# Kernel tuning notes

Measured on AMD Instinct MI355X. Metric: run time of the kernel, lower is better.

Reference implementation:

```python
import jax, jax.numpy as jnp
import numpy as np

P, K, H, D = 64, 8, 32, 2048   # ids_per_batch, imgs_per_id, local stripes, feature dim
MARGIN = 10.0


def _euclid(x, y):
    # x: [m, d], y: [n, d] -> [m, n]
    xx = jnp.sum(x * x, axis=1, keepdims=True)          # [m, 1]
    yy = jnp.sum(y * y, axis=1)[None, :]                # [1, n]
    d2 = xx + yy - 2.0 * (x @ y.T)
    return jnp.sqrt(jnp.clip(d2, 1e-12, None))


def _shortest_dist(dmat):
    # dmat: [m, n, *rest]; DP: dist[i,j] = dmat[i,j] + min(dist[i-1,j], dist[i,j-1])
    m, n = dmat.shape[0], dmat.shape[1]
    rest = dmat.shape[2:]
    d = dmat.reshape(m, n, -1)                          # [m, n, B]
    B = d.shape[2]
    # virtual row above: +inf everywhere except col 0 (so dist[0,0] = dmat[0,0])
    prev0 = jnp.full((n, B), jnp.inf, d.dtype).at[0].set(0.0)

    def row_step(prev_row, drow):
        def col_step(left, ud):
            up, dd = ud
            cur = jnp.minimum(up, left) + dd
            return cur, cur
        _, row = jax.lax.scan(col_step, jnp.full((B,), jnp.inf, d.dtype), (prev_row, drow))
        return row, None

    last_row, _ = jax.lax.scan(row_step, prev0, d)
    return last_row[-1].reshape(rest)                   # dist at (m-1, n-1)


def _local_dist(x, y):
    # x: [M, m, d], y: [N, n, d] -> [M, N]
    M, m, d = x.shape
    N, n, _ = y.shape
    dm = _euclid(x.reshape(M * m, d), y.reshape(N * n, d))
    dm = jnp.tanh(dm * 0.5)                             # (e^d - 1) / (e^d + 1)
    dm = dm.reshape(M, m, N, n).transpose(1, 3, 0, 2)   # [m, n, M, N]
    return _shortest_dist(dm)                           # [M, N]


def setup_inputs() -> dict:
    key = jax.random.key(0)
    features = jax.random.normal(key, (P * K, H, D), dtype=jnp.float32)
    targets = jnp.arange(P * K, dtype=jnp.int32) // K   # ordered p*k labels
    return {"features": features, "targets": targets}


def reference(features, targets):
    # ordered p*k batch: classes are contiguous blocks of K
    feats = features.reshape(P, K, H, D)
    centers = feats.mean(axis=1)                        # [P, H, D]

    # intra: center vs its K members -> max over members, per class
    intra_max = jax.vmap(lambda c, f: _local_dist(c[None], f).max())(centers, feats)  # [P]

    # inter: center vs all other centers -> min over others, per class
    inter_full = _local_dist(centers, centers)          # [P, P]
    eye = jnp.eye(P, dtype=bool)
    inter_min = jnp.where(eye, jnp.inf, inter_full).min(axis=1)  # [P]

    loss = jnp.mean(jax.nn.relu(intra_max - inter_min + MARGIN))
    return loss, intra_max, inter_min
```

## Files before the change

kernel.cpp:

```cpp
#include <hip/hip_runtime.h>
#include <hip/hip_fp8.h>
#include <cstdint>
#include <cstddef>

#define PP 64
#define KK 8
#define HH 32
#define DD 2048
#define RR (PP*HH)

typedef __attribute__((ext_vector_type(4))) float  f32x4;
typedef __attribute__((ext_vector_type(4))) float  float4v;

__device__ __forceinline__ unsigned int f2fp8(float f) {
  return (unsigned int)__hip_fp8_e4m3(f).__x;
}

__device__ __forceinline__ void gload_lds16(const void* g, void* l) {
  __builtin_amdgcn_global_load_lds(
      (const __attribute__((address_space(1))) void*)g,
      (__attribute__((address_space(3))) void*)l, 16, 0, 0);
}

__device__ __forceinline__ void gload_lds16_nt(const void* g, void* l) {
  __builtin_amdgcn_global_load_lds(
      (const __attribute__((address_space(1))) void*)g,
      (__attribute__((address_space(3))) void*)l, 16, 0, 2);
}

__device__ __forceinline__ float dp_wave(const float* tile, int j32) {
  const float INF = __builtin_inff();
  float A = INF;
  for (int d = 0; d < 63; ++d) {
    float left = __shfl_up(A, 1, 32);
    if (j32 == 0) left = INF;
    int i = d - j32;
    int ii = i < 0 ? 0 : (i > 31 ? 31 : i);
    float dv = tile[(ii << 5) + j32];
    float up = (i == 0) ? (j32 == 0 ? 0.f : INF) : A;
    A = (i >= 0 && i < 32) ? (fminf(up, left) + dv) : INF;
  }
  return A;
}

__global__ __launch_bounds__(256) void k_centers(const float* __restrict__ feat,
    unsigned char* __restrict__ cbf, unsigned char* __restrict__ fbf,
    float* __restrict__ cnorm, float* __restrict__ fnorm) {
  int row = blockIdx.x;
  int p = row >> 5, h = row & 31;
  int tid = threadIdx.x;
  int d0 = tid * 8;
  float c[8];
  float red[9];
  #pragma unroll
  for (int e = 0; e < 8; ++e) c[e] = 0.f;
  #pragma unroll
  for (int k = 0; k < KK; ++k) {
    size_t frow = (size_t)((p*KK + k)*HH + h);
    const float* src = feat + frow*DD + d0;
    float4v f0 = *(const float4v*)src;
    float4v f1 = *(const float4v*)(src + 4);
    float s = 0.f;
    #pragma unroll
    for (int e = 0; e < 4; ++e) {
      c[e]   += f0[e];
      c[4+e] += f1[e];
      s += f0[e]*f0[e] + f1[e]*f1[e];
    }
    red[k] = s;
    unsigned int lo = f2fp8(f0[0]) | (f2fp8(f0[1])<<8) | (f2fp8(f0[2])<<16) | (f2fp8(f0[3])<<24);
    unsigned int hi = f2fp8(f1[0]) | (f2fp8(f1[1])<<8) | (f2fp8(f1[2])<<16) | (f2fp8(f1[3])<<24);
    *(uint2*)(fbf + frow*DD + d0) = make_uint2(lo, hi);
  }
  float csq = 0.f;
  #pragma unroll
  for (int e = 0; e < 8; ++e) { c[e] *= 0.125f; csq += c[e]*c[e]; }
  {
    unsigned int lo = f2fp8(c[0]) | (f2fp8(c[1])<<8) | (f2fp8(c[2])<<16) | (f2fp8(c[3])<<24);
    unsigned int hi = f2fp8(c[4]) | (f2fp8(c[5])<<8) | (f2fp8(c[6])<<16) | (f2fp8(c[7])<<24);
    *(uint2*)(cbf + (size_t)row*DD + d0) = make_uint2(lo, hi);
  }
  red[8] = csq;

  __shared__ float lred[4][9];
  int lane = tid & 63, wv = tid >> 6;
  #pragma unroll
  for (int r = 0; r < 9; ++r) {
    float v = red[r];
    #pragma unroll
    for (int off = 32; off > 0; off >>= 1) v += __shfl_down(v, off, 64);
    if (lane == 0) lred[wv][r] = v;
  }
  __syncthreads();
  if (tid < 9) {
    float s = lred[0][tid] + lred[1][tid] + lred[2][tid] + lred[3][tid];
    if (tid < 8) fnorm[((size_t)(p*KK + tid))*HH + h] = s;
    else         cnorm[row] = s;
  }
}

__global__ __launch_bounds__(256) void k_gram(const unsigned char* __restrict__ cbf,
    const unsigned char* __restrict__ fbf, const float* __restrict__ cnorm,
    const float* __restrict__ fnorm, float* __restrict__ inter_full,
    float* __restrict__ intra_pk) {
  __shared__ char smem[24576];
  int tid = threadIdx.x, lane = tid & 63, w = tid >> 6;
  int ln = lane & 15, kq = lane >> 4;
  int cch = (lane & 3) ^ ((lane >> 3) & 3);

  if (blockIdx.x < 528) {
    int bid = (blockIdx.x & 7)*66 + (blockIdx.x >> 3);
    int tI = 0, rem = bid;
    while (rem >= 32 - tI) { rem -= 32 - tI; ++tI; }
    int tJ = tI + rem;
    int wr = w >> 1, wc = w & 1;
    f32x4 acc[2][2];
    #pragma unroll
    for (int a = 0; a < 2; ++a)
      #pragma unroll
      for (int b = 0; b < 2; ++b)
        #pragma unroll
        for (int e = 0; e < 4; ++e) acc[a][b][e] = 0.f;

    const unsigned char* gA0 = cbf + (size_t)(tI*64 + w*16 + (lane >> 2))*DD + cch*16;
    const unsigned char* gB0 = cbf + (size_t)(tJ*64 + w*16 + (lane >> 2))*DD + cch*16;

    int aofs[2][2], bofs[2][2];
    #pragma unroll
    for (int ks = 0; ks < 2; ++ks) {
      int phys = ((ks*4 + kq) ^ (ln & 6))*8;
      #pragma unroll
      for (int mt = 0; mt < 2; ++mt) {
        aofs[ks][mt] = (wr*32 + mt*16 + ln)*64 + phys;
        bofs[ks][mt] = (wc*32 + mt*16 + ln)*64 + phys;
      }
    }

    auto stage = [&](int tt, int bi) {
      int k0 = tt * 64;
      char* A = smem + bi*8192;
      gload_lds16(gA0 + k0, A + w*1024 + lane*16);
      gload_lds16(gB0 + k0, A + 4096 + w*1024 + lane*16);
    };
    auto do_step = [&](int bi) {
      const char* A = smem + bi*8192;
      const char* B = A + 4096;
      #pragma unroll
      for (int ks = 0; ks < 2; ++ks) {
        long long af[2], bf[2];
        #pragma unroll
        for (int mt = 0; mt < 2; ++mt) {
          af[mt] = *(const long long*)(A + aofs[ks][mt]);
          bf[mt] = *(const long long*)(B + bofs[ks][mt]);
        }
        #pragma unroll
        for (int mt = 0; mt < 2; ++mt)
          #pragma unroll
          for (int nt = 0; nt < 2; ++nt)
            acc[mt][nt] = __builtin_amdgcn_mfma_f32_16x16x32_fp8_fp8(af[mt], bf[nt], acc[mt][nt], 0, 0, 0);
      }
    };

    stage(0, 0);
    stage(1, 1);
    asm volatile("s_waitcnt vmcnt(2)" ::: "memory");
    __builtin_amdgcn_s_barrier();
    for (int t = 0; t < 30; ++t) {
      stage(t + 2, (t + 2) % 3);
      do_step(t % 3);
      asm volatile("s_waitcnt vmcnt(2)" ::: "memory");
      __builtin_amdgcn_s_barrier();
    }
    do_step(0);
    asm volatile("s_waitcnt vmcnt(0)" ::: "memory");
    __builtin_amdgcn_s_barrier();
    do_step(1);
    __syncthreads();

    int a = tI*2 + wr, b = tJ*2 + wc;
    bool own = (a < b);
    float* tile = (float*)(smem + w*4096);
    if (own) {
      #pragma unroll
      for (int mt = 0; mt < 2; ++mt) {
        #pragma unroll
        for (int nt = 0; nt < 2; ++nt) {
          int j  = nt*16 + ln;
          int cc = tJ*64 + wc*32 + j;
          float nc = cnorm[cc];
          #pragma unroll
          for (int v = 0; v < 4; ++v) {
            int i  = mt*16 + kq*4 + v;
            int rr = tI*64 + wr*32 + i;
            float d2 = cnorm[rr] + nc - 2.f*acc[mt][nt][v];
            tile[(i << 5) + j] = tanhf(0.5f*sqrtf(fmaxf(d2, 1e-12f)));
          }
        }
      }
    }
    __syncthreads();
    if (own) {
      float A = dp_wave(tile, lane & 31);
      if (lane == 31) {
        inter_full[a*64 + b] = A;
        inter_full[b*64 + a] = A;
      }
    }
  } else {
    int bid = (int)blockIdx.x - 528;
    int p = bid >> 3, jb = bid & 7;
    int ks = w >> 1, nt = w & 1;
    f32x4 acc[2];
    #pragma unroll
    for (int mi = 0; mi < 2; ++mi)
      #pragma unroll
      for (int e = 0; e < 4; ++e) acc[mi][e] = 0.f;

    int hw = w & 1;
    const unsigned char* g0 = (w < 2)
        ? cbf + (size_t)(p*32 + hw*16 + (lane >> 2))*DD + cch*16
        : fbf + (size_t)(p*256 + jb*32 + hw*16 + (lane >> 2))*DD + cch*16;
    int isB = (w >= 2);

    int phys = ((ks*4 + kq) ^ (ln & 6))*8;
    int aofs[2];
    #pragma unroll
    for (int mi = 0; mi < 2; ++mi) aofs[mi] = (mi*16 + ln)*64 + phys;
    int bofs = (nt*16 + ln)*64 + phys;

    auto stage = [&](int tt, int bi) {
      int k0 = tt * 64;
      char* S = smem + bi*4096 + isB*2048;
      if (isB) gload_lds16_nt(g0 + k0, S + hw*1024 + lane*16);
      else     gload_lds16   (g0 + k0, S + hw*1024 + lane*16);
    };
    auto do_step = [&](int bi) {
      const char* A = smem + bi*4096;
      const char* B = A + 2048;
      long long bfr = *(const long long*)(B + bofs);
      #pragma unroll
      for (int mi = 0; mi < 2; ++mi) {
        long long af = *(const long long*)(A + aofs[mi]);
        acc[mi] = __builtin_amdgcn_mfma_f32_16x16x32_fp8_fp8(af, bfr, acc[mi], 0, 0, 0);
      }
    };

    stage(0, 0);
    stage(1, 1);
    asm volatile("s_waitcnt vmcnt(1)" ::: "memory");
    __builtin_amdgcn_s_barrier();
    for (int t = 0; t < 30; ++t) {
      stage(t + 2, (t + 2) % 3);
      do_step(t % 3);
      asm volatile("s_waitcnt vmcnt(1)" ::: "memory");
      __builtin_amdgcn_s_barrier();
    }
    do_step(0);
    asm volatile("s_waitcnt vmcnt(0)" ::: "memory");
    __builtin_amdgcn_s_barrier();
    do_step(1);

    float* fb = (float*)smem;
    float* tile = (float*)(smem + 16384);
    __syncthreads();
    if (w >= 2) {
      #pragma unroll
      for (int mi = 0; mi < 2; ++mi)
        *(f32x4*)(fb + ((w - 2)*2 + mi)*256 + lane*4) = acc[mi];
    }
    __syncthreads();
    if (w < 2) {
      #pragma unroll
      for (int mi = 0; mi < 2; ++mi)
        acc[mi] += *(const f32x4*)(fb + (w*2 + mi)*256 + lane*4);
      int cl = jb*32 + nt*16 + ln;
      float nf = fnorm[(size_t)p*256 + cl];
      #pragma unroll
      for (int mi = 0; mi < 2; ++mi) {
        #pragma unroll
        for (int v = 0; v < 4; ++v) {
          int i = mi*16 + kq*4 + v;
          float d2 = cnorm[p*32 + i] + nf - 2.f*acc[mi][v];
          tile[(i << 5) + (nt*16 + ln)] = tanhf(0.5f*sqrtf(fmaxf(d2, 1e-12f)));
        }
      }
    }
    __syncthreads();
    if (w == 0) {
      float A = dp_wave(tile, lane & 31);
      if (lane == 31) intra_pk[p*8 + jb] = A;
    }
  }
}

__global__ __launch_bounds__(64) void k_final(const float* __restrict__ inter_full,
    const float* __restrict__ intra_pk, float* __restrict__ out) {
  int p = threadIdx.x;
  const float INF = __builtin_inff();
  float mn = INF;
  #pragma unroll 8
  for (int b = 0; b < 64; ++b)
    if (b != p) mn = fminf(mn, inter_full[p*64 + b]);
  float mx = -INF;
  #pragma unroll
  for (int k = 0; k < 8; ++k) mx = fmaxf(mx, intra_pk[p*8 + k]);
  out[1 + p]  = mx;
  out[65 + p] = mn;
  float v = fmaxf(mx - mn + 10.0f, 0.0f);
  #pragma unroll
  for (int off = 32; off > 0; off >>= 1) v += __shfl_down(v, off, 64);
  if (p == 0) out[0] = v * (1.0f/64.0f);
}

extern "C" void kernel_launch(void* const* d_in, const int* in_sizes, int n_in,
                              void* d_out, int out_size, void* d_ws, size_t ws_size,
                              hipStream_t stream) {
  const float* feat = (const float*)d_in[0];
  float* out = (float*)d_out;
  char* w = (char*)d_ws;
  unsigned char* cbf  = (unsigned char*)w;
  unsigned char* fbf  = (unsigned char*)(w + 4194304);
  float* cnorm        = (float*)(w + 37748736);
  float* fnorm        = (float*)(w + 37756928);
  float* inter_full   = (float*)(w + 37822464);
  float* intra_pk     = (float*)(w + 37838848);

  k_centers<<<RR, 256, 0, stream>>>(feat, cbf, fbf, cnorm, fnorm);
  k_gram<<<1040, 256, 0, stream>>>(cbf, fbf, cnorm, fnorm, inter_full, intra_pk);
  k_final<<<1, 64, 0, stream>>>(inter_full, intra_pk, out);
}
```

Measured before the change: 73.11 us.

## Merge gram blocks into 512-thread blocks sharing the A tile across two column tiles

Each inter block now computes two adjacent column tiles (tJ pairs) in 512 threads, loading the row-tile A once into LDS and sharing it across both halves, so the amount of A data fetched from global memory drops. The intra blocks are also doubled up, each 512-thread block handling two (p, jb) jobs in separate LDS regions. The nontemporal load variant for feature data is dropped. The grid shrinks from 1040 to 528 blocks with a larger LDS footprint per block, which may reduce occupancy. Larger blocks also mean more waves waiting at each barrier.

```diff
diff --git a/kernel.cpp b/kernel.cpp
--- a/kernel.cpp
+++ b/kernel.cpp
@@ -20,12 +20,6 @@
   __builtin_amdgcn_global_load_lds(
       (const __attribute__((address_space(1))) void*)g,
       (__attribute__((address_space(3))) void*)l, 16, 0, 0);
-}
-
-__device__ __forceinline__ void gload_lds16_nt(const void* g, void* l) {
-  __builtin_amdgcn_global_load_lds(
-      (const __attribute__((address_space(1))) void*)g,
-      (__attribute__((address_space(3))) void*)l, 16, 0, 2);
 }
 
 __device__ __forceinline__ float dp_wave(const float* tile, int j32) {
@@ -99,21 +93,24 @@
   }
 }
 
-__global__ __launch_bounds__(256) void k_gram(const unsigned char* __restrict__ cbf,
+__global__ __launch_bounds__(512) void k_gram(const unsigned char* __restrict__ cbf,
     const unsigned char* __restrict__ fbf, const float* __restrict__ cnorm,
     const float* __restrict__ fnorm, float* __restrict__ inter_full,
     float* __restrict__ intra_pk) {
-  __shared__ char smem[24576];
+  __shared__ char smem[40960];
   int tid = threadIdx.x, lane = tid & 63, w = tid >> 6;
   int ln = lane & 15, kq = lane >> 4;
   int cch = (lane & 3) ^ ((lane >> 3) & 3);
 
-  if (blockIdx.x < 528) {
-    int bid = (blockIdx.x & 7)*66 + (blockIdx.x >> 3);
+  int xcd = blockIdx.x & 7, idx = blockIdx.x >> 3;
+  if (idx < 34) {
+    int bid = xcd*34 + idx;
     int tI = 0, rem = bid;
-    while (rem >= 32 - tI) { rem -= 32 - tI; ++tI; }
-    int tJ = tI + rem;
-    int wr = w >> 1, wc = w & 1;
+    while (rem >= 16 - (tI >> 1)) { rem -= 16 - (tI >> 1); ++tI; }
+    int tJp = (tI >> 1) + rem;
+    int jh = w >> 2, q = w & 3;
+    int wr = q >> 1, wc = q & 1;
+    int tJ = tJp*2 + jh;
     f32x4 acc[2][2];
     #pragma unroll
     for (int a = 0; a < 2; ++a)
@@ -122,8 +119,21 @@
         #pragma unroll
         for (int e = 0; e < 4; ++e) acc[a][b][e] = 0.f;
 
-    const unsigned char* gA0 = cbf + (size_t)(tI*64 + w*16 + (lane >> 2))*DD + cch*16;
-    const unsigned char* gB0 = cbf + (size_t)(tJ*64 + w*16 + (lane >> 2))*DD + cch*16;
+    const unsigned char* g0;
+    const unsigned char* g1 = nullptr;
+    int d0ofs = 0, d1ofs = 0;
+    int role2 = (w >= 4);
+    if (!role2) {
+      g0 = cbf + (size_t)(tI*64 + w*16 + (lane >> 2))*DD + cch*16;
+      d0ofs = w*1024 + lane*16;
+    } else {
+      int j = w - 4, jB = j >> 1, half = j & 1;
+      int tJj = tJp*2 + jB;
+      g0 = cbf + (size_t)(tJj*64 + half*32 + (lane >> 2))*DD + cch*16;
+      g1 = g0 + (size_t)16*DD;
+      d0ofs = 4096 + jB*4096 + half*2048 + lane*16;
+      d1ofs = d0ofs + 1024;
+    }
 
     int aofs[2][2], bofs[2][2];
     #pragma unroll
@@ -132,26 +142,25 @@
       #pragma unroll
       for (int mt = 0; mt < 2; ++mt) {
         aofs[ks][mt] = (wr*32 + mt*16 + ln)*64 + phys;
-        bofs[ks][mt] = (wc*32 + mt*16 + ln)*64 + phys;
+        bofs[ks][mt] = 4096 + jh*4096 + (wc*32 + mt*16 + ln)*64 + phys;
       }
     }
 
     auto stage = [&](int tt, int bi) {
       int k0 = tt * 64;
-      char* A = smem + bi*8192;
-      gload_lds16(gA0 + k0, A + w*1024 + lane*16);
-      gload_lds16(gB0 + k0, A + 4096 + w*1024 + lane*16);
+      char* buf = smem + bi*12288;
+      gload_lds16(g0 + k0, buf + d0ofs);
+      if (role2) gload_lds16(g1 + k0, buf + d1ofs);
     };
     auto do_step = [&](int bi) {
-      const char* A = smem + bi*8192;
-      const char* B = A + 4096;
+      const char* buf = smem + bi*12288;
       #pragma unroll
       for (int ks = 0; ks < 2; ++ks) {
         long long af[2], bf[2];
         #pragma unroll
         for (int mt = 0; mt < 2; ++mt) {
-          af[mt] = *(const long long*)(A + aofs[ks][mt]);
-          bf[mt] = *(const long long*)(B + bofs[ks][mt]);
+          af[mt] = *(const long long*)(buf + aofs[ks][mt]);
+          bf[mt] = *(const long long*)(buf + bofs[ks][mt]);
         }
         #pragma unroll
         for (int mt = 0; mt < 2; ++mt)
@@ -163,12 +172,14 @@
 
     stage(0, 0);
     stage(1, 1);
-    asm volatile("s_waitcnt vmcnt(2)" ::: "memory");
+    if (!role2) { asm volatile("s_waitcnt vmcnt(1)" ::: "memory"); }
+    else        { asm volatile("s_waitcnt vmcnt(2)" ::: "memory"); }
     __builtin_amdgcn_s_barrier();
     for (int t = 0; t < 30; ++t) {
       stage(t + 2, (t + 2) % 3);
       do_step(t % 3);
-      asm volatile("s_waitcnt vmcnt(2)" ::: "memory");
+      if (!role2) { asm volatile("s_waitcnt vmcnt(1)" ::: "memory"); }
+      else        { asm volatile("s_waitcnt vmcnt(2)" ::: "memory"); }
       __builtin_amdgcn_s_barrier();
     }
     do_step(0);
@@ -207,20 +218,24 @@
       }
     }
   } else {
-    int bid = (int)blockIdx.x - 528;
-    int p = bid >> 3, jb = bid & 7;
-    int ks = w >> 1, nt = w & 1;
+    int bid = xcd*32 + (idx - 34);
+    int u  = w >> 2;
+    int wu = w & 3;
+    int rb = u * 20480;
+    int qq = bid*2 + u;
+    int p = qq >> 3, jb = qq & 7;
+    int ks = wu >> 1, nt = wu & 1;
     f32x4 acc[2];
     #pragma unroll
     for (int mi = 0; mi < 2; ++mi)
       #pragma unroll
       for (int e = 0; e < 4; ++e) acc[mi][e] = 0.f;
 
-    int hw = w & 1;
-    const unsigned char* g0 = (w < 2)
+    int hw = wu & 1;
+    const unsigned char* g0 = (wu < 2)
         ? cbf + (size_t)(p*32 + hw*16 + (lane >> 2))*DD + cch*16
         : fbf + (size_t)(p*256 + jb*32 + hw*16 + (lane >> 2))*DD + cch*16;
-    int isB = (w >= 2);
+    int isB = (wu >= 2);
 
     int phys = ((ks*4 + kq) ^ (ln & 6))*8;
     int aofs[2];
@@ -230,12 +245,11 @@
 
     auto stage = [&](int tt, int bi) {
       int k0 = tt * 64;
-      char* S = smem + bi*4096 + isB*2048;
-      if (isB) gload_lds16_nt(g0 + k0, S + hw*1024 + lane*16);
-      else     gload_lds16   (g0 + k0, S + hw*1024 + lane*16);
+      char* S = smem + rb + bi*4096 + isB*2048;
+      gload_lds16(g0 + k0, S + hw*1024 + lane*16);
     };
     auto do_step = [&](int bi) {
-      const char* A = smem + bi*4096;
+      const char* A = smem + rb + bi*4096;
       const char* B = A + 2048;
       long long bfr = *(const long long*)(B + bofs);
       #pragma unroll
@@ -260,19 +274,19 @@
     __builtin_amdgcn_s_barrier();
     do_step(1);
 
-    float* fb = (float*)smem;
-    float* tile = (float*)(smem + 16384);
-    __syncthreads();
-    if (w >= 2) {
+    float* fb = (float*)(smem + rb);
+    float* tile = (float*)(smem + rb + 16384);
+    __syncthreads();
+    if (wu >= 2) {
       #pragma unroll
       for (int mi = 0; mi < 2; ++mi)
-        *(f32x4*)(fb + ((w - 2)*2 + mi)*256 + lane*4) = acc[mi];
-    }
-    __syncthreads();
-    if (w < 2) {
+        *(f32x4*)(fb + ((wu - 2)*2 + mi)*256 + lane*4) = acc[mi];
+    }
+    __syncthreads();
+    if (wu < 2) {
       #pragma unroll
       for (int mi = 0; mi < 2; ++mi)
-        acc[mi] += *(const f32x4*)(fb + (w*2 + mi)*256 + lane*4);
+        acc[mi] += *(const f32x4*)(fb + (wu*2 + mi)*256 + lane*4);
       int cl = jb*32 + nt*16 + ln;
       float nf = fnorm[(size_t)p*256 + cl];
       #pragma unroll
@@ -286,7 +300,7 @@
       }
     }
     __syncthreads();
-    if (w == 0) {
+    if (wu == 0) {
       float A = dp_wave(tile, lane & 31);
       if (lane == 31) intra_pk[p*8 + jb] = A;
     }
@@ -326,6 +340,6 @@
   float* intra_pk     = (float*)(w + 37838848);
 
   k_centers<<<RR, 256, 0, stream>>>(feat, cbf, fbf, cnorm, fnorm);
-  k_gram<<<1040, 256, 0, stream>>>(cbf, fbf, cnorm, fnorm, inter_full, intra_pk);
+  k_gram<<<528, 512, 0, stream>>>(cbf, fbf, cnorm, fnorm, inter_full, intra_pk);
   k_final<<<1, 64, 0, stream>>>(inter_full, intra_pk, out);
 }
```

Result: faster. 68.59 us (-6.2%).
